# Optimization experiments

Measured on AMD Instinct MI355X. Metric: run time of the kernel, lower is better.

Reference implementation:

```python
import jax, jax.numpy as jnp
import numpy as np

D_MODEL = 2048
N_HEADS = 16
HEAD_DIM = D_MODEL // N_HEADS


def setup_inputs() -> dict:
    key = jax.random.key(0)
    k_x, k_wqkv, k_bqkv, k_wo, k_bo = jax.random.split(key, 5)
    B, T = 4, 1024
    s_in = 1.0 / np.sqrt(D_MODEL)
    return {
        "x": jax.random.normal(k_x, (B, T, D_MODEL), dtype=jnp.float32),
        "w_qkv": jax.random.uniform(k_wqkv, (D_MODEL, 3 * D_MODEL), jnp.float32, -s_in, s_in),
        "b_qkv": jax.random.uniform(k_bqkv, (3 * D_MODEL,), jnp.float32, -s_in, s_in),
        "w_out": jax.random.uniform(k_wo, (D_MODEL, D_MODEL), jnp.float32, -s_in, s_in),
        "b_out": jax.random.uniform(k_bo, (D_MODEL,), jnp.float32, -s_in, s_in),
    }


def reference(x, w_qkv, b_qkv, w_out, b_out) -> jnp.ndarray:
    B, T, C = x.shape
    qkv = x @ w_qkv + b_qkv                      # [B, T, 3C]
    q, k, v = jnp.split(qkv, 3, axis=-1)
    # [B, H, T, Dh]
    q = q.reshape(B, T, N_HEADS, HEAD_DIM).transpose(0, 2, 1, 3)
    k = k.reshape(B, T, N_HEADS, HEAD_DIM).transpose(0, 2, 1, 3)
    v = v.reshape(B, T, N_HEADS, HEAD_DIM).transpose(0, 2, 1, 3)
    scale = 1.0 / np.sqrt(HEAD_DIM).astype(np.float32)
    att = jnp.einsum("bhqd,bhkd->bhqk", q, k) * scale   # [B, H, T, T]
    causal = jnp.tril(jnp.ones((T, T), dtype=bool))
    att = jnp.where(causal, att, -jnp.inf)
    att = jax.nn.softmax(att, axis=-1)
    out = jnp.einsum("bhqk,bhkd->bhqd", att, v)          # [B, H, T, Dh]
    out = out.transpose(0, 2, 1, 3).reshape(B, T, C)
    return out @ w_out + b_out
```

## Files before the change

### kernel.cpp

```cpp
#include <hip/hip_runtime.h>
#include <hip/hip_bf16.h>
#include <math.h>

#define DM    2048
#define DQKV  6144
#define NH    16
#define DH    128
#define TT    1024
#define BB    4

typedef __bf16 bf16_t;
typedef __bf16 bf16x4 __attribute__((ext_vector_type(4)));
typedef __bf16 bf16x8 __attribute__((ext_vector_type(8)));
typedef float  f32x4  __attribute__((ext_vector_type(4)));

__device__ __forceinline__ void async16(const void* g, void* lds) {
  __builtin_amdgcn_global_load_lds(
      (const __attribute__((address_space(1))) unsigned int*)g,
      (__attribute__((address_space(3))) unsigned int*)lds, 16, 0, 0);
}

__device__ __forceinline__ void block_barrier() {
  asm volatile("" ::: "memory");
  __builtin_amdgcn_s_barrier();
  asm volatile("" ::: "memory");
}

__global__ __launch_bounds__(256) void cast_kernel(const float* __restrict__ X,
                                                   bf16_t* __restrict__ Xb) {
  const size_t i = ((size_t)blockIdx.x * 256 + threadIdx.x) * 8;
  float4 a = *(const float4*)(X + i);
  float4 b = *(const float4*)(X + i + 4);
  bf16x8 o = {(bf16_t)a.x, (bf16_t)a.y, (bf16_t)a.z, (bf16_t)a.w,
              (bf16_t)b.x, (bf16_t)b.y, (bf16_t)b.z, (bf16_t)b.w};
  *(bf16x8*)(Xb + i) = o;
}

__global__ __launch_bounds__(256) void transpose_cast_kernel(
    const float* __restrict__ W, bf16_t* __restrict__ Wt, int K, int N) {
  __shared__ bf16_t tile[64][72];
  const int tid = threadIdx.x;
  const int tk = blockIdx.y * 64, tn = blockIdx.x * 64;
  {
    int r = tid >> 2, c0 = (tid & 3) * 16;
    const float* src = W + (size_t)(tk + r) * N + tn + c0;
#pragma unroll
    for (int j = 0; j < 4; ++j) {
      float4 v = *(const float4*)(src + j * 4);
      tile[r][c0 + j * 4 + 0] = (bf16_t)v.x;
      tile[r][c0 + j * 4 + 1] = (bf16_t)v.y;
      tile[r][c0 + j * 4 + 2] = (bf16_t)v.z;
      tile[r][c0 + j * 4 + 3] = (bf16_t)v.w;
    }
  }
  __syncthreads();
  {
    int n = tid >> 2, c0 = (tid & 3) * 16;
    bf16_t* dst = Wt + (size_t)(tn + n) * K + tk + c0;
#pragma unroll
    for (int j = 0; j < 4; ++j) {
      bf16x4 t = {tile[c0 + j * 4 + 0][n], tile[c0 + j * 4 + 1][n],
                  tile[c0 + j * 4 + 2][n], tile[c0 + j * 4 + 3][n]};
      *(bf16x4*)(dst + j * 4) = t;
    }
  }
}

__global__ __launch_bounds__(256) void v_transpose_kernel(
    const bf16_t* __restrict__ qkv, bf16_t* __restrict__ Vt_g) {
  __shared__ bf16_t tile[64][72];
  const int tid = threadIdx.x;
  const int dt = blockIdx.x;
  const int tt = blockIdx.y;
  const int bh = blockIdx.z;
  const int b = bh >> 4, h = bh & 15;
  {
    int r = tid >> 2, c0 = (tid & 3) * 16;
    const bf16_t* src =
        qkv + (size_t)(b * TT + tt * 64 + r) * DQKV + 2 * DM + h * DH + dt * 64 + c0;
    *(bf16x8*)&tile[r][c0]     = *(const bf16x8*)(src);
    *(bf16x8*)&tile[r][c0 + 8] = *(const bf16x8*)(src + 8);
  }
  __syncthreads();
  {
    int n = tid >> 2, c0 = (tid & 3) * 16;
    bf16_t* dst = Vt_g + (size_t)(bh * DH + dt * 64 + n) * TT + tt * 64 + c0;
#pragma unroll
    for (int j = 0; j < 4; ++j) {
      bf16x4 t = {tile[c0 + j * 4 + 0][n], tile[c0 + j * 4 + 1][n],
                  tile[c0 + j * 4 + 2][n], tile[c0 + j * 4 + 3][n]};
      *(bf16x4*)(dst + j * 4) = t;
    }
  }
}

template <bool OUT_BF16, int BCH>
__global__ __launch_bounds__(512, 2) void gemm_big_kernel(
    const bf16_t* __restrict__ A, const bf16_t* __restrict__ Bt,
    const float* __restrict__ bias, void* __restrict__ out,
    int M, int N, int K, int nbm) {
  __shared__ __align__(16) bf16_t As[2][256 * 64];
  __shared__ __align__(16) bf16_t Bs[2][BCH * 64 * 64];

  const int tid  = threadIdx.x;
  const int lane = tid & 63;
  const int wave = tid >> 6;
  const int ln   = lane & 15;
  const int quad = lane >> 4;

  const int cpx = gridDim.x >> 3;
  const int wg  = (blockIdx.x & 7) * cpx + (blockIdx.x >> 3);
  const int bm  = wg & (nbm - 1);
  const int bn  = wg / nbm;

  const bf16_t* Abase = A + (size_t)bm * 256 * K;
  const bf16_t* Bbase = Bt + (size_t)bn * (BCH * 64) * K;

  const int m0 = (wave >> 2) * 128;
  const int n0 = (wave & 3) * (BCH * 16);

  f32x4 acc[8][BCH] = {};

  const int NT = K >> 6;

  auto stageA = [&](int kt, int d) {
#pragma unroll
    for (int s = 0; s < 4; ++s) {
      const int fb  = s * 512 + wave * 64;
      const int f   = fb + lane;
      const int row = f >> 3, c = f & 7;
      const int gc  = c ^ (row & 7);
      async16(Abase + (size_t)row * K + kt * 64 + gc * 8,
              (char*)(&As[d][0]) + fb * 16);
    }
  };
  auto stageB = [&](int kt, int d) {
#pragma unroll
    for (int s = 0; s < BCH; ++s) {
      const int fb  = s * 512 + wave * 64;
      const int f   = fb + lane;
      const int row = f >> 3, c = f & 7;
      const int gc  = c ^ (row & 7);
      async16(Bbase + (size_t)row * K + kt * 64 + gc * 8,
              (char*)(&Bs[d][0]) + fb * 16);
    }
  };
  auto vm_lpt = [&] {
    if constexpr (BCH == 3)
      asm volatile("s_waitcnt vmcnt(7)" ::: "memory");
    else
      asm volatile("s_waitcnt vmcnt(6)" ::: "memory");
  };

  stageA(0, 0);
  stageB(0, 0);
  stageA(1, 1);
  stageB(1, 1);
  vm_lpt();
  block_barrier();

  for (int kt = 0; kt < NT; ++kt) {
    const int cur = kt & 1;

    bf16x8 af[8][2], bfr[BCH][2];
#pragma unroll
    for (int ks = 0; ks < 2; ++ks) {
#pragma unroll
      for (int i = 0; i < 8; ++i) {
        const int row = m0 + 16 * i + ln;
        const int c = (ks * 4 + quad) ^ (row & 7);
        af[i][ks] =
            *(const bf16x8*)((const char*)(&As[cur][0]) + ((row * 8 + c) << 4));
      }
#pragma unroll
      for (int j = 0; j < BCH; ++j) {
        const int row = n0 + 16 * j + ln;
        const int c = (ks * 4 + quad) ^ (row & 7);
        bfr[j][ks] =
            *(const bf16x8*)((const char*)(&Bs[cur][0]) + ((row * 8 + c) << 4));
      }
    }
    asm volatile("s_waitcnt lgkmcnt(0)" ::: "memory");
    block_barrier();

    if (kt + 2 < NT) stageA(kt + 2, cur);
    __builtin_amdgcn_s_setprio(1);
#pragma unroll
    for (int i = 0; i < 8; ++i)
#pragma unroll
      for (int j = 0; j < BCH; ++j)
        acc[i][j] = __builtin_amdgcn_mfma_f32_16x16x32_bf16(af[i][0], bfr[j][0],
                                                            acc[i][j], 0, 0, 0);
    __builtin_amdgcn_s_setprio(0);
    if (kt + 2 < NT) stageB(kt + 2, cur);
    __builtin_amdgcn_s_setprio(1);
#pragma unroll
    for (int i = 0; i < 8; ++i)
#pragma unroll
      for (int j = 0; j < BCH; ++j)
        acc[i][j] = __builtin_amdgcn_mfma_f32_16x16x32_bf16(af[i][1], bfr[j][1],
                                                            acc[i][j], 0, 0, 0);
    __builtin_amdgcn_s_setprio(0);

    if (kt + 2 < NT)
      vm_lpt();
    else
      asm volatile("s_waitcnt vmcnt(0)" ::: "memory");
    block_barrier();
  }

#pragma unroll
  for (int i = 0; i < 8; ++i) {
    const int rowg = bm * 256 + m0 + 16 * i + quad * 4;
#pragma unroll
    for (int j = 0; j < BCH; ++j) {
      const int colg = bn * (BCH * 64) + n0 + 16 * j + ln;
      const float bb = bias[colg];
#pragma unroll
      for (int r = 0; r < 4; ++r) {
        float val = acc[i][j][r] + bb;
        if (OUT_BF16)
          ((bf16_t*)out)[(size_t)(rowg + r) * N + colg] = (bf16_t)val;
        else
          ((float*)out)[(size_t)(rowg + r) * N + colg] = val;
      }
    }
  }
}

__global__ __launch_bounds__(256, 2) void attn_kernel(
    const bf16_t* __restrict__ qkv, const bf16_t* __restrict__ Vt_g,
    bf16_t* __restrict__ attout) {
  const int bx = blockIdx.x;
  const int bh = bx & 63;
  const int j_  = bx >> 6;
  const int rr  = j_ >> 2, cc_ = j_ & 3;
  const int qt  = (rr & 1) ? (rr * 4 + (3 - cc_)) : (rr * 4 + cc_);
  const int b  = bh >> 4;
  const int h  = bh & 15;
  const int tid  = threadIdx.x;
  const int lane = tid & 63;
  const int wave = tid >> 6;
  const int ln   = lane & 15;
  const int quad = lane >> 4;

  __shared__ __align__(16) bf16_t Ks[2][64 * 128];
  __shared__ __align__(16) bf16_t Vs[2][128 * 64];
  __shared__ __align__(16) bf16_t Ps[4 * 16 * 64];

  const float scale = 0.08838834764831845f;
  const float SHIFT = 12.0f;
  const int q0 = qt * 64 + wave * 16;

  bf16x8 aq[4];
  {
    const bf16_t* qrow = qkv + (size_t)(b * TT + q0 + ln) * DQKV + h * DH;
#pragma unroll
    for (int kt = 0; kt < 4; ++kt)
      aq[kt] = *(const bf16x8*)(qrow + kt * 32 + quad * 8);
  }

  auto stage = [&](int c, int buf) {
    const int kc = c * 64;
#pragma unroll
    for (int j = 0; j < 4; ++j) {
      const int fb = j * 256 + wave * 64;
      const int l  = fb + lane;
      {
        const int row = l >> 4, cc = l & 15;
        const int gc  = cc ^ (row & 7);
        const bf16_t* g =
            qkv + (size_t)(b * TT + kc + row) * DQKV + DM + h * DH + gc * 8;
        async16(g, (char*)(&Ks[buf][0]) + fb * 16);
      }
      {
        const int d = l >> 3, cc = l & 7;
        const int gc = cc ^ (d & 7);
        const bf16_t* g = Vt_g + (size_t)(bh * DH + d) * TT + kc + gc * 8;
        async16(g, (char*)(&Vs[buf][0]) + fb * 16);
      }
    }
  };

  f32x4 o[8] = {};
  float lp[4] = {0.f, 0.f, 0.f, 0.f};

  stage(0, 0);

  for (int c = 0; c <= qt; ++c) {
    const int cur = c & 1;
    const char* Kc = (const char*)(&Ks[cur][0]);
    const char* Vc = (const char*)(&Vs[cur][0]);

    asm volatile("s_waitcnt lgkmcnt(0)" ::: "memory");
    block_barrier();
    if (c < qt) {
      stage(c + 1, cur ^ 1);
      asm volatile("s_waitcnt vmcnt(8)" ::: "memory");
    } else {
      asm volatile("s_waitcnt vmcnt(0)" ::: "memory");
    }
    block_barrier();

    f32x4 sacc[4];
    __builtin_amdgcn_s_setprio(1);
#pragma unroll
    for (int jt = 0; jt < 4; ++jt) {
      sacc[jt] = (f32x4){0.f, 0.f, 0.f, 0.f};
#pragma unroll
      for (int kt = 0; kt < 4; ++kt) {
        const int row = jt * 16 + ln;
        const int sc  = (kt * 4 + quad) ^ (row & 7);
        bf16x8 bk = *(const bf16x8*)(Kc + row * 256 + sc * 16);
        sacc[jt] = __builtin_amdgcn_mfma_f32_16x16x32_bf16(aq[kt], bk,
                                                           sacc[jt], 0, 0, 0);
      }
    }
    __builtin_amdgcn_s_setprio(0);

    const int kc = c * 64;
    const bool diag = (c == qt);
#pragma unroll
    for (int jt = 0; jt < 4; ++jt) {
      const int colg = kc + jt * 16 + ln;
#pragma unroll
      for (int r = 0; r < 4; ++r) {
        float sv = sacc[jt][r] * scale - SHIFT;
        if (diag && colg > q0 + quad * 4 + r) sv = -1e30f;
        float pv = __expf(sv);
        lp[r] += pv;
        const int row = quad * 4 + r;
        const int col = jt * 16 + ln;
        const int sc  = (col >> 3) ^ (row & 7);
        Ps[wave * 1024 + row * 64 + sc * 8 + (col & 7)] = (bf16_t)pv;
      }
    }

    __builtin_amdgcn_s_setprio(1);
#pragma unroll
    for (int ks = 0; ks < 2; ++ks) {
      const int psc = (ks * 4 + quad) ^ (ln & 7);
      bf16x8 ap =
          *(const bf16x8*)((const char*)Ps + wave * 2048 + ln * 128 + psc * 16);
#pragma unroll
      for (int nt = 0; nt < 8; ++nt) {
        const int row = nt * 16 + ln;
        const int sc  = (ks * 4 + quad) ^ (row & 7);
        bf16x8 bv = *(const bf16x8*)(Vc + row * 128 + sc * 16);
        o[nt] = __builtin_amdgcn_mfma_f32_16x16x32_bf16(ap, bv, o[nt], 0, 0, 0);
      }
    }
    __builtin_amdgcn_s_setprio(0);
  }

#pragma unroll
  for (int off = 1; off < 16; off <<= 1)
#pragma unroll
    for (int r = 0; r < 4; ++r) lp[r] += __shfl_xor(lp[r], off, 64);

#pragma unroll
  for (int r = 0; r < 4; ++r) {
    float inv = 1.0f / lp[r];
    int t = q0 + quad * 4 + r;
    bf16_t* orow = attout + (size_t)(b * TT + t) * DM + h * DH;
#pragma unroll
    for (int nt = 0; nt < 8; ++nt)
      orow[nt * 16 + ln] = (bf16_t)(o[nt][r] * inv);
  }
}

extern "C" void kernel_launch(void* const* d_in, const int* in_sizes, int n_in,
                              void* d_out, int out_size, void* d_ws,
                              size_t ws_size, hipStream_t stream) {
  const float* x     = (const float*)d_in[0];
  const float* w_qkv = (const float*)d_in[1];
  const float* b_qkv = (const float*)d_in[2];
  const float* w_out = (const float*)d_in[3];
  const float* b_out = (const float*)d_in[4];
  float* out = (float*)d_out;

  char* ws = (char*)d_ws;
  bf16_t* qkv    = (bf16_t*)(ws);
  bf16_t* wqkv_t = (bf16_t*)(ws + 50331648);
  bf16_t* Vt_g   = wqkv_t;
  bf16_t* wout_t = (bf16_t*)(ws + 75497472);
  bf16_t* xb     = (bf16_t*)(ws + 83886080);
  bf16_t* attout = xb;

  dim3 blk(256);
  cast_kernel<<<dim3(4096), blk, 0, stream>>>(x, xb);
  transpose_cast_kernel<<<dim3(96, 32), blk, 0, stream>>>(w_qkv, wqkv_t, 2048, 6144);
  transpose_cast_kernel<<<dim3(32, 32), blk, 0, stream>>>(w_out, wout_t, 2048, 2048);
  gemm_big_kernel<true, 3><<<dim3(256), dim3(512), 0, stream>>>(
      xb, wqkv_t, b_qkv, qkv, 2048, 6144, 2048, 8);
  gemm_big_kernel<true, 3><<<dim3(256), dim3(512), 0, stream>>>(
      xb + (size_t)2048 * 2048, wqkv_t, b_qkv, qkv + (size_t)2048 * 6144,
      2048, 6144, 2048, 8);
  v_transpose_kernel<<<dim3(2, 16, 64), blk, 0, stream>>>(qkv, Vt_g);
  attn_kernel<<<dim3(1024), blk, 0, stream>>>(qkv, Vt_g, attout);
  gemm_big_kernel<false, 2><<<dim3(256), dim3(512), 0, stream>>>(
      attout, wout_t, b_out, out, 4096, 2048, 2048, 16);
}
```

Measured before the change: 340.2 us.

## Merge prep kernels, single QKV GEMM launch, fuse V transpose into epilogue

```diff
diff --git a/kernel.cpp b/kernel.cpp
--- a/kernel.cpp
+++ b/kernel.cpp
@@ -26,21 +26,34 @@
   asm volatile("" ::: "memory");
 }
 
-__global__ __launch_bounds__(256) void cast_kernel(const float* __restrict__ X,
-                                                   bf16_t* __restrict__ Xb) {
-  const size_t i = ((size_t)blockIdx.x * 256 + threadIdx.x) * 8;
-  float4 a = *(const float4*)(X + i);
-  float4 b = *(const float4*)(X + i + 4);
-  bf16x8 o = {(bf16_t)a.x, (bf16_t)a.y, (bf16_t)a.z, (bf16_t)a.w,
-              (bf16_t)b.x, (bf16_t)b.y, (bf16_t)b.z, (bf16_t)b.w};
-  *(bf16x8*)(Xb + i) = o;
-}
-
-__global__ __launch_bounds__(256) void transpose_cast_kernel(
-    const float* __restrict__ W, bf16_t* __restrict__ Wt, int K, int N) {
+__global__ __launch_bounds__(256) void prep_kernel(
+    const float* __restrict__ x, bf16_t* __restrict__ xb,
+    const float* __restrict__ w_qkv, bf16_t* __restrict__ wqkv_t,
+    const float* __restrict__ w_out, bf16_t* __restrict__ wout_t) {
+  const int tid = threadIdx.x;
+  const int bx = blockIdx.x;
+  if (bx < 4096) {
+    const size_t i = ((size_t)bx * 256 + tid) * 8;
+    float4 a = *(const float4*)(x + i);
+    float4 b = *(const float4*)(x + i + 4);
+    bf16x8 o = {(bf16_t)a.x, (bf16_t)a.y, (bf16_t)a.z, (bf16_t)a.w,
+                (bf16_t)b.x, (bf16_t)b.y, (bf16_t)b.z, (bf16_t)b.w};
+    *(bf16x8*)(xb + i) = o;
+    return;
+  }
   __shared__ bf16_t tile[64][72];
-  const int tid = threadIdx.x;
-  const int tk = blockIdx.y * 64, tn = blockIdx.x * 64;
+  const float* W;
+  bf16_t* Wt;
+  int K, N, tn, tk;
+  if (bx < 7168) {
+    const int t = bx - 4096;
+    W = w_qkv; Wt = wqkv_t; K = 2048; N = 6144;
+    tn = (t % 96) * 64; tk = (t / 96) * 64;
+  } else {
+    const int t = bx - 7168;
+    W = w_out; Wt = wout_t; K = 2048; N = 2048;
+    tn = (t % 32) * 64; tk = (t / 32) * 64;
+  }
   {
     int r = tid >> 2, c0 = (tid & 3) * 16;
     const float* src = W + (size_t)(tk + r) * N + tn + c0;
@@ -94,11 +107,11 @@
   }
 }
 
-template <bool OUT_BF16, int BCH>
+template <bool OUT_BF16, int BCH, bool WRITE_VT>
 __global__ __launch_bounds__(512, 2) void gemm_big_kernel(
     const bf16_t* __restrict__ A, const bf16_t* __restrict__ Bt,
     const float* __restrict__ bias, void* __restrict__ out,
-    int M, int N, int K, int nbm) {
+    bf16_t* __restrict__ vt, int M, int N, int K, int nbm) {
   __shared__ __align__(16) bf16_t As[2][256 * 64];
   __shared__ __align__(16) bf16_t Bs[2][BCH * 64 * 64];
 
@@ -214,15 +227,23 @@
     const int rowg = bm * 256 + m0 + 16 * i + quad * 4;
 #pragma unroll
     for (int j = 0; j < BCH; ++j) {
-      const int colg = bn * (BCH * 64) + n0 + 16 * j + ln;
+      const int cb   = bn * (BCH * 64) + n0 + 16 * j;
+      const int colg = cb + ln;
       const float bb = bias[colg];
-#pragma unroll
-      for (int r = 0; r < 4; ++r) {
-        float val = acc[i][j][r] + bb;
-        if (OUT_BF16)
-          ((bf16_t*)out)[(size_t)(rowg + r) * N + colg] = (bf16_t)val;
-        else
-          ((float*)out)[(size_t)(rowg + r) * N + colg] = val;
+      if (WRITE_VT && cb >= 2 * DM) {
+        const int vrow = ((rowg >> 10) << 11) + (colg - 2 * DM);
+        bf16x4 v = {(bf16_t)(acc[i][j][0] + bb), (bf16_t)(acc[i][j][1] + bb),
+                    (bf16_t)(acc[i][j][2] + bb), (bf16_t)(acc[i][j][3] + bb)};
+        *(bf16x4*)(vt + (size_t)vrow * TT + (rowg & (TT - 1))) = v;
+      } else {
+#pragma unroll
+        for (int r = 0; r < 4; ++r) {
+          float val = acc[i][j][r] + bb;
+          if (OUT_BF16)
+            ((bf16_t*)out)[(size_t)(rowg + r) * N + colg] = (bf16_t)val;
+          else
+            ((float*)out)[(size_t)(rowg + r) * N + colg] = val;
+        }
       }
     }
   }
@@ -382,22 +403,24 @@
   char* ws = (char*)d_ws;
   bf16_t* qkv    = (bf16_t*)(ws);
   bf16_t* wqkv_t = (bf16_t*)(ws + 50331648);
-  bf16_t* Vt_g   = wqkv_t;
   bf16_t* wout_t = (bf16_t*)(ws + 75497472);
   bf16_t* xb     = (bf16_t*)(ws + 83886080);
   bf16_t* attout = xb;
 
-  dim3 blk(256);
-  cast_kernel<<<dim3(4096), blk, 0, stream>>>(x, xb);
-  transpose_cast_kernel<<<dim3(96, 32), blk, 0, stream>>>(w_qkv, wqkv_t, 2048, 6144);
-  transpose_cast_kernel<<<dim3(32, 32), blk, 0, stream>>>(w_out, wout_t, 2048, 2048);
-  gemm_big_kernel<true, 3><<<dim3(256), dim3(512), 0, stream>>>(
-      xb, wqkv_t, b_qkv, qkv, 2048, 6144, 2048, 8);
-  gemm_big_kernel<true, 3><<<dim3(256), dim3(512), 0, stream>>>(
-      xb + (size_t)2048 * 2048, wqkv_t, b_qkv, qkv + (size_t)2048 * 6144,
-      2048, 6144, 2048, 8);
-  v_transpose_kernel<<<dim3(2, 16, 64), blk, 0, stream>>>(qkv, Vt_g);
-  attn_kernel<<<dim3(1024), blk, 0, stream>>>(qkv, Vt_g, attout);
-  gemm_big_kernel<false, 2><<<dim3(256), dim3(512), 0, stream>>>(
-      attout, wout_t, b_out, out, 4096, 2048, 2048, 16);
-}
+  const bool fuse_vt = (ws_size >= 117440512);
+  bf16_t* Vt_g = fuse_vt ? (bf16_t*)(ws + 100663296) : wqkv_t;
+
+  prep_kernel<<<dim3(8192), dim3(256), 0, stream>>>(x, xb, w_qkv, wqkv_t,
+                                                    w_out, wout_t);
+  if (fuse_vt) {
+    gemm_big_kernel<true, 3, true><<<dim3(512), dim3(512), 0, stream>>>(
+        xb, wqkv_t, b_qkv, qkv, Vt_g, 4096, 6144, 2048, 16);
+  } else {
+    gemm_big_kernel<true, 3, false><<<dim3(512), dim3(512), 0, stream>>>(
+        xb, wqkv_t, b_qkv, qkv, nullptr, 4096, 6144, 2048, 16);
+    v_transpose_kernel<<<dim3(2, 16, 64), dim3(256), 0, stream>>>(qkv, Vt_g);
+  }
+  attn_kernel<<<dim3(1024), dim3(256), 0, stream>>>(qkv, Vt_g, attout);
+  gemm_big_kernel<false, 2, false><<<dim3(256), dim3(512), 0, stream>>>(
+      attout, wout_t, b_out, out, nullptr, 4096, 2048, 2048, 16);
+}
```

New measurement: 329.9 us, median of 2. 3.0% less time.
